# Optimization experiments

Hardware: AMD Instinct MI355X
Metric: run time of the kernel (lower is better)

Reference implementation:

```python
import jax, jax.numpy as jnp
import numpy as np
import math

B, L, D, H = 8, 1000, 1024, 16
HD = D // H

def setup_inputs() -> dict:
    key = jax.random.key(0)
    k1, k2, k3 = jax.random.split(key, 3)
    s_in = 1.0 / math.sqrt(D)
    x = jax.random.normal(k1, (B, L, D), dtype=jnp.float32)
    Wqkv = jax.random.normal(k2, (D, 3 * D), dtype=jnp.float32) * s_in
    bqkv = jnp.zeros((3 * D,), dtype=jnp.float32)
    Wo = jax.random.normal(k3, (D, D), dtype=jnp.float32) * s_in
    bo = jnp.zeros((D,), dtype=jnp.float32)
    return {"x": x, "Wqkv": Wqkv, "bqkv": bqkv, "Wo": Wo, "bo": bo}

def reference(x, Wqkv, bqkv, Wo, bo):
    b, l, d = x.shape
    qkv = x @ Wqkv + bqkv                      # [B,L,3D]
    q, k, v = jnp.split(qkv, 3, axis=-1)       # each [B,L,D]
    q = q.reshape(b, l, H, HD)
    k = k.reshape(b, l, H, HD)
    v = v.reshape(b, l, H, HD)
    scale = 1.0 / math.sqrt(HD)
    att = jnp.einsum('blhd,bmhd->bhlm', q, k) * scale   # [B,H,L,L]
    causal = jnp.tril(jnp.ones((l, l), dtype=bool))      # [L,L]
    att = jnp.where(causal[None, None, :, :], att, -jnp.inf)
    att = jax.nn.softmax(att, axis=-1)
    out = jnp.einsum('bhlm,bmhd->blhd', att, v).reshape(b, l, d)
    return out @ Wo + bo
```

## Files before the change

kernel.cpp:

```cpp
#include <hip/hip_runtime.h>
#include <hip/hip_bf16.h>

typedef unsigned short u16;
typedef unsigned int u32;
typedef __attribute__((ext_vector_type(8))) __bf16 bf16x8;
typedef __attribute__((ext_vector_type(4))) float f32x4;
typedef __attribute__((ext_vector_type(4))) u16 u16x4;

#define LQ 1000
#define MM 8000

__device__ __forceinline__ u16 f2bf(float f){
  __bf16 h = (__bf16)f;
  return __builtin_bit_cast(u16, h);
}
__device__ __forceinline__ void async_copy16(const void* g, void* l){
  __builtin_amdgcn_global_load_lds((const __attribute__((address_space(1))) u32*)g,
                                   (__attribute__((address_space(3))) u32*)l, 16, 0, 0);
}

__global__ __launch_bounds__(256)
void kcvt(const float* __restrict__ src, u16* __restrict__ dst, long n){
  const long i = ((long)blockIdx.x * 256 + threadIdx.x) * 4;
  if (i + 3 >= n) {
    for (long j = i; j < n; j++) dst[j] = f2bf(src[j]);
    return;
  }
  const float4 v = *(const float4*)&src[i];
  u16x4 o; o.x = f2bf(v.x); o.y = f2bf(v.y); o.z = f2bf(v.z); o.w = f2bf(v.w);
  *(u16x4*)&dst[i] = o;
}

__global__ __launch_bounds__(256)
void ktranspose_cvt(const float* __restrict__ src, u16* __restrict__ dst, int R, int C){
  __shared__ u16 tile[32][33];
  const int tx = threadIdx.x & 31, ty = threadIdx.x >> 5;
  const long bx = (long)blockIdx.x * 32, by = (long)blockIdx.y * 32;
  #pragma unroll
  for (int i = 0; i < 32; i += 8) tile[ty + i][tx] = f2bf(src[(by + ty + i) * C + bx + tx]);
  __syncthreads();
  #pragma unroll
  for (int i = 0; i < 32; i += 8) dst[(bx + ty + i) * R + by + tx] = tile[tx][ty + i];
}

template<int EPI>
__global__ __launch_bounds__(512, 2)
void gemm256(const u16* __restrict__ A, const u16* __restrict__ BT, const float* __restrict__ bias,
             u16* __restrict__ O0, u16* __restrict__ O1, u16* __restrict__ O2,
             float* __restrict__ OF)
{
  constexpr int K = 1024;
  constexpr int NT = K / 32;
  extern __shared__ __align__(16) char lds[];
  const int t = threadIdx.x, lane = t & 63, wave = t >> 6;
  const int quad = lane >> 4, l15 = lane & 15;

  const int nwgx = gridDim.x;
  const int nwg = nwgx * gridDim.y;
  int bid = blockIdx.y * nwgx + blockIdx.x;
  bid = (bid & 7) * (nwg >> 3) + (bid >> 3);
  const int m0 = (bid / nwgx) * 256, n0 = (bid % nwgx) * 256;

  const int wm = (wave >> 2) * 128, wn = (wave & 3) * 64;

  const int srow  = wave * 16 + (lane >> 2);
  const int scolg = (lane & 3) ^ ((srow >> 1) & 3);
  const long aofs0 = (long)min(m0 + srow,       MM - 1) * K + scolg * 8;
  const long aofs1 = (long)min(m0 + srow + 128, MM - 1) * K + scolg * 8;
  const long bofs0 = (long)(n0 + srow)       * K + scolg * 8;
  const long bofs1 = (long)(n0 + srow + 128) * K + scolg * 8;

  const int swz = (l15 >> 1) & 3;
  int aoff[8], boff[4];
  #pragma unroll
  for (int m = 0; m < 8; m++) aoff[m] = (wm + m * 16 + l15) * 64 + ((quad ^ swz) << 4);
  #pragma unroll
  for (int n = 0; n < 4; n++) boff[n] = 16384 + (wn + n * 16 + l15) * 64 + ((quad ^ swz) << 4);

  f32x4 acc[8][4] = {};

  auto STAGE_A = [&](int j){
    char* d = lds + (j & 3) * 32768 + wave * 1024;
    const long kt = (long)j * 32;
    async_copy16(A + aofs0 + kt, d);
    async_copy16(A + aofs1 + kt, d + 8192);
  };
  auto STAGE_B = [&](int j){
    char* d = lds + (j & 3) * 32768 + 16384 + wave * 1024;
    const long kt = (long)j * 32;
    async_copy16(BT + bofs0 + kt, d);
    async_copy16(BT + bofs1 + kt, d + 8192);
  };

  STAGE_A(0); STAGE_B(0);
  STAGE_A(1); STAGE_B(1);
  STAGE_A(2); STAGE_B(2);

  for (int j = 0; j < NT; ++j) {
    if (j < NT - 2)       asm volatile("s_waitcnt vmcnt(8)" ::: "memory");
    else if (j == NT - 2) asm volatile("s_waitcnt vmcnt(4)" ::: "memory");
    else                  asm volatile("s_waitcnt vmcnt(0)" ::: "memory");
    __builtin_amdgcn_s_barrier();

    char* buf = lds + (j & 3) * 32768;
    bf16x8 bfr[4], afr[4];
    #pragma unroll
    for (int n = 0; n < 4; n++) bfr[n] = *(const bf16x8*)(buf + boff[n]);
    #pragma unroll
    for (int m = 0; m < 4; m++) afr[m] = *(const bf16x8*)(buf + aoff[m]);
    if (j < NT - 3) STAGE_A(j + 3);

    __builtin_amdgcn_s_setprio(1);
    #pragma unroll
    for (int m = 0; m < 4; m++)
      #pragma unroll
      for (int n = 0; n < 4; n++)
        acc[m][n] = __builtin_amdgcn_mfma_f32_16x16x32_bf16(afr[m], bfr[n], acc[m][n], 0, 0, 0);
    __builtin_amdgcn_s_setprio(0);
    __builtin_amdgcn_s_barrier();

    #pragma unroll
    for (int m = 0; m < 4; m++) afr[m] = *(const bf16x8*)(buf + aoff[m + 4]);
    if (j < NT - 3) STAGE_B(j + 3);

    __builtin_amdgcn_s_setprio(1);
    #pragma unroll
    for (int m = 0; m < 4; m++)
      #pragma unroll
      for (int n = 0; n < 4; n++)
        acc[m + 4][n] = __builtin_amdgcn_mfma_f32_16x16x32_bf16(afr[m], bfr[n], acc[m + 4][n], 0, 0, 0);
    __builtin_amdgcn_s_setprio(0);

    asm volatile("s_waitcnt lgkmcnt(0)" ::: "memory");
  }

  float bs[4]; int cols[4];
  #pragma unroll
  for (int n = 0; n < 4; n++) { cols[n] = n0 + wn + n * 16 + l15; bs[n] = bias[cols[n]]; }

  #pragma unroll
  for (int m = 0; m < 8; m++) {
    #pragma unroll
    for (int r = 0; r < 4; r++) {
      const int row = m0 + wm + m * 16 + quad * 4 + r;
      if (row >= MM) continue;
      if (EPI == 0) {
        const int b = row / 1000, l = row - b * 1000;
        #pragma unroll
        for (int n = 0; n < 4; n++) {
          const u16 o = f2bf(acc[m][n][r] + bs[n]);
          const int col = cols[n];
          const int which = col >> 10, hh = (col >> 6) & 15, dd = col & 63;
          const int bh = b * 16 + hh;
          if      (which == 0) O0[((long)bh * LQ + l) * 64 + dd] = o;
          else if (which == 1) O1[((long)bh * LQ + l) * 64 + dd] = o;
          else                 O2[((long)bh * 64 + dd) * LQ + l] = o;
        }
      } else {
        #pragma unroll
        for (int n = 0; n < 4; n++)
          OF[(long)row * 1024 + cols[n]] = acc[m][n][r] + bs[n];
      }
    }
  }
}

__global__ __launch_bounds__(256)
void attn_kernel(const u16* __restrict__ Qb, const u16* __restrict__ Kb,
                 const u16* __restrict__ VTb, u16* __restrict__ AO)
{
  __shared__ __align__(16) u16 Ps[4][2][16 * 40];
  const int t = threadIdx.x, lane = t & 63, wave = t >> 6;
  const int quad = lane >> 4, l15 = lane & 15;
  const int bh = blockIdx.y;
  const int c = blockIdx.x * 4 + wave;
  const u16* Q  = Qb  + (long)bh * LQ * 64;
  const u16* Kp = Kb  + (long)bh * LQ * 64;
  const u16* VT = VTb + (long)bh * 64 * LQ;
  const int b = bh >> 4, h = bh & 15;
  const float sscale = 0.18033688011112042f;

  for (int pass = 0; pass < 2; ++pass) {
    const int chunk = pass ? (31 - c) : c;
    const int qbase = chunk * 32;
    const int nkt = chunk + 1;

    int qv[2]; bf16x8 bq0[2], bq1[2];
    #pragma unroll
    for (int g = 0; g < 2; g++) {
      qv[g] = qbase + g * 16 + l15;
      const int qc = min(qv[g], LQ - 1);
      bq0[g] = *(const bf16x8*)&Q[(long)qc * 64 +      quad * 8];
      bq1[g] = *(const bf16x8*)&Q[(long)qc * 64 + 32 + quad * 8];
    }

    float l_p[2] = { 0.f, 0.f };
    f32x4 o[2][4] = {};

    bf16x8 pa00, pa01, pa10, pa11, pav0, pav1, pav2, pav3;
    {
      const int krA = min(l15, LQ - 1), krB = min(16 + l15, LQ - 1);
      pa00 = *(const bf16x8*)&Kp[(long)krA * 64 +      quad * 8];
      pa01 = *(const bf16x8*)&Kp[(long)krA * 64 + 32 + quad * 8];
      pa10 = *(const bf16x8*)&Kp[(long)krB * 64 +      quad * 8];
      pa11 = *(const bf16x8*)&Kp[(long)krB * 64 + 32 + quad * 8];
      const int vcol = min(quad * 8, LQ - 8);
      pav0 = *(const bf16x8*)&VT[(long)( 0 + l15) * LQ + vcol];
      pav1 = *(const bf16x8*)&VT[(long)(16 + l15) * LQ + vcol];
      pav2 = *(const bf16x8*)&VT[(long)(32 + l15) * LQ + vcol];
      pav3 = *(const bf16x8*)&VT[(long)(48 + l15) * LQ + vcol];
    }

    for (int kk = 0; kk < nkt; ++kk) {
      const int k0 = kk * 32;
      const bool lastt = (kk + 1 == nkt);
      const bf16x8 a00 = pa00, a01 = pa01, a10 = pa10, a11 = pa11;
      bf16x8 av[4] = { pav0, pav1, pav2, pav3 };
      if (!lastt) {
        const int n0k = k0 + 32;
        const int krA = min(n0k + l15, LQ - 1), krB = min(n0k + 16 + l15, LQ - 1);
        pa00 = *(const bf16x8*)&Kp[(long)krA * 64 +      quad * 8];
        pa01 = *(const bf16x8*)&Kp[(long)krA * 64 + 32 + quad * 8];
        pa10 = *(const bf16x8*)&Kp[(long)krB * 64 +      quad * 8];
        pa11 = *(const bf16x8*)&Kp[(long)krB * 64 + 32 + quad * 8];
        const int vcol = min(n0k + quad * 8, LQ - 8);
        pav0 = *(const bf16x8*)&VT[(long)( 0 + l15) * LQ + vcol];
        pav1 = *(const bf16x8*)&VT[(long)(16 + l15) * LQ + vcol];
        pav2 = *(const bf16x8*)&VT[(long)(32 + l15) * LQ + vcol];
        pav3 = *(const bf16x8*)&VT[(long)(48 + l15) * LQ + vcol];
      }

      #pragma unroll
      for (int g = 0; g < 2; g++) {
        const f32x4 z = {};
        f32x4 s0 = __builtin_amdgcn_mfma_f32_16x16x32_bf16(a00, bq0[g], z, 0, 0, 0);
        s0       = __builtin_amdgcn_mfma_f32_16x16x32_bf16(a01, bq1[g], s0, 0, 0, 0);
        f32x4 s1 = __builtin_amdgcn_mfma_f32_16x16x32_bf16(a10, bq0[g], z, 0, 0, 0);
        s1       = __builtin_amdgcn_mfma_f32_16x16x32_bf16(a11, bq1[g], s1, 0, 0, 0);

        float p0[4], p1[4];
        if (lastt) {
          const int q = qv[g];
          #pragma unroll
          for (int r = 0; r < 4; r++) {
            const int key0 = k0 + quad * 4 + r;
            p0[r] = __builtin_amdgcn_exp2f((key0      <= q) ? s0[r] * sscale : -3.0e38f);
            p1[r] = __builtin_amdgcn_exp2f((key0 + 16 <= q) ? s1[r] * sscale : -3.0e38f);
          }
        } else {
          #pragma unroll
          for (int r = 0; r < 4; r++) {
            p0[r] = __builtin_amdgcn_exp2f(s0[r] * sscale);
            p1[r] = __builtin_amdgcn_exp2f(s1[r] * sscale);
          }
        }
        u16x4 w0, w1; float ls = 0.f;
        #pragma unroll
        for (int r = 0; r < 4; r++) {
          w0[r] = f2bf(p0[r]); w1[r] = f2bf(p1[r]);
          ls += p0[r] + p1[r];
        }
        l_p[g] += ls;
        *(u16x4*)&Ps[wave][g][l15 * 40 + quad * 4]      = w0;
        *(u16x4*)&Ps[wave][g][l15 * 40 + 16 + quad * 4] = w1;
        const bf16x8 bp = *(const bf16x8*)&Ps[wave][g][l15 * 40 + quad * 8];
        #pragma unroll
        for (int cc = 0; cc < 4; cc++)
          o[g][cc] = __builtin_amdgcn_mfma_f32_16x16x32_bf16(av[cc], bp, o[g][cc], 0, 0, 0);
      }
    }

    #pragma unroll
    for (int g = 0; g < 2; g++) {
      if (qv[g] >= LQ) continue;
      float l = l_p[g];
      l += __shfl_xor(l, 16);
      l += __shfl_xor(l, 32);
      const float inv = 1.0f / l;
      const long base = ((long)(b * LQ + qv[g])) * 1024 + h * 64;
      #pragma unroll
      for (int cc = 0; cc < 4; cc++) {
        u16x4 w;
        #pragma unroll
        for (int r = 0; r < 4; r++) w[r] = f2bf(o[g][cc][r] * inv);
        *(u16x4*)&AO[base + cc * 16 + quad * 4] = w;
      }
    }
  }
}

extern "C" void kernel_launch(void* const* d_in, const int* in_sizes, int n_in,
                              void* d_out, int out_size, void* d_ws, size_t ws_size,
                              hipStream_t stream) {
  const float* x    = (const float*)d_in[0];
  const float* Wqkv = (const float*)d_in[1];
  const float* bqkv = (const float*)d_in[2];
  const float* Wo   = (const float*)d_in[3];
  const float* bo   = (const float*)d_in[4];
  float* out = (float*)d_out;

  char* ws = (char*)d_ws;
  u16* WqkvT = (u16*)(ws);
  u16* WoT   = (u16*)(ws + 6291456);
  u16* xb    = (u16*)(ws + 8388608);
  u16* Qb    = (u16*)(ws + 8388608 + 16384000L);
  u16* Kb    = (u16*)(ws + 8388608 + 2 * 16384000L);
  u16* VTb   = (u16*)(ws + 8388608 + 3 * 16384000L);
  u16* AO    = xb;

  static bool inited = false;
  if (!inited) {
    (void)hipFuncSetAttribute(reinterpret_cast<const void*>(&gemm256<0>),
                              hipFuncAttributeMaxDynamicSharedMemorySize, 131072);
    (void)hipFuncSetAttribute(reinterpret_cast<const void*>(&gemm256<1>),
                              hipFuncAttributeMaxDynamicSharedMemorySize, 131072);
    inited = true;
  }

  kcvt<<<8000, 256, 0, stream>>>(x, xb, 8192000L);
  ktranspose_cvt<<<dim3(96, 32), 256, 0, stream>>>(Wqkv, WqkvT, 1024, 3072);
  ktranspose_cvt<<<dim3(32, 32), 256, 0, stream>>>(Wo,   WoT,   1024, 1024);
  gemm256<0><<<dim3(12, 32), 512, 131072, stream>>>(xb, WqkvT, bqkv, Qb, Kb, VTb, nullptr);
  attn_kernel<<<dim3(4, 128), 256, 0, stream>>>(Qb, Kb, VTb, AO);
  gemm256<1><<<dim3(4, 32), 512, 131072, stream>>>(AO, WoT, bo, nullptr, nullptr, nullptr, out);
}
```

Baseline: 276.0 us.

## Template GEMM on N tile, use 256x128 tiles for output projection, restructure barriers

The GEMM kernel gets a template parameter for N tile width. The output projection now runs with 256x128 tiles, doubling its grid from 128 to 256 workgroups so more of the GPU's compute units have work. The main loop is reorganised so the vmcnt wait sits at the end of each iteration, with extra barriers pinned by sched_barrier between the LDS fragment loads and the MFMA phases. The extra barriers per iteration may add synchronisation cost, and the smaller B tile gives less reuse per loaded A tile.

```diff
diff --git a/kernel.cpp b/kernel.cpp
--- a/kernel.cpp
+++ b/kernel.cpp
@@ -17,6 +17,17 @@
 __device__ __forceinline__ void async_copy16(const void* g, void* l){
   __builtin_amdgcn_global_load_lds((const __attribute__((address_space(1))) u32*)g,
                                    (__attribute__((address_space(3))) u32*)l, 16, 0, 0);
+}
+template<int N> __device__ __forceinline__ void wait_vm(){
+  if constexpr (N==8)      asm volatile("s_waitcnt vmcnt(8)" ::: "memory");
+  else if constexpr (N==6) asm volatile("s_waitcnt vmcnt(6)" ::: "memory");
+  else if constexpr (N==4) asm volatile("s_waitcnt vmcnt(4)" ::: "memory");
+  else if constexpr (N==3) asm volatile("s_waitcnt vmcnt(3)" ::: "memory");
+  else                     asm volatile("s_waitcnt vmcnt(0)" ::: "memory");
+}
+__device__ __forceinline__ void barrier_pin(){
+  asm volatile("s_barrier" ::: "memory");
+  __builtin_amdgcn_sched_barrier(0);
 }
 
 __global__ __launch_bounds__(256)
@@ -43,14 +54,16 @@
   for (int i = 0; i < 32; i += 8) dst[(bx + ty + i) * R + by + tx] = tile[tx][ty + i];
 }
 
-template<int EPI>
+template<int EPI, int BN>
 __global__ __launch_bounds__(512, 2)
-void gemm256(const u16* __restrict__ A, const u16* __restrict__ BT, const float* __restrict__ bias,
-             u16* __restrict__ O0, u16* __restrict__ O1, u16* __restrict__ O2,
-             float* __restrict__ OF)
+void gemm8p(const u16* __restrict__ A, const u16* __restrict__ BT, const float* __restrict__ bias,
+            u16* __restrict__ O0, u16* __restrict__ O1, u16* __restrict__ O2,
+            float* __restrict__ OF)
 {
-  constexpr int K = 1024;
-  constexpr int NT = K / 32;
+  constexpr int K = 1024, NT = K / 32;
+  constexpr int NF = BN / 64;
+  constexpr int BUFSZ = 16384 + BN * 64;
+  constexpr int PT = 2 + BN / 128;
   extern __shared__ __align__(16) char lds[];
   const int t = threadIdx.x, lane = t & 63, wave = t >> 6;
   const int quad = lane >> 4, l15 = lane & 15;
@@ -59,84 +72,82 @@
   const int nwg = nwgx * gridDim.y;
   int bid = blockIdx.y * nwgx + blockIdx.x;
   bid = (bid & 7) * (nwg >> 3) + (bid >> 3);
-  const int m0 = (bid / nwgx) * 256, n0 = (bid % nwgx) * 256;
-
-  const int wm = (wave >> 2) * 128, wn = (wave & 3) * 64;
-
-  const int srow  = wave * 16 + (lane >> 2);
-  const int scolg = (lane & 3) ^ ((srow >> 1) & 3);
-  const long aofs0 = (long)min(m0 + srow,       MM - 1) * K + scolg * 8;
-  const long aofs1 = (long)min(m0 + srow + 128, MM - 1) * K + scolg * 8;
-  const long bofs0 = (long)(n0 + srow)       * K + scolg * 8;
-  const long bofs1 = (long)(n0 + srow + 128) * K + scolg * 8;
+  const int m0 = (bid / nwgx) * 256, n0 = (bid % nwgx) * BN;
+
+  const int wm = (wave >> 2) * 128, wn = (wave & 3) * (BN / 4);
+
+  const int srow = t >> 2;
+  const int sg   = (t & 3) ^ ((srow >> 1) & 3);
+  const long aofs0 = (long)min(m0 + srow,       MM - 1) * K + sg * 8;
+  const long aofs1 = (long)min(m0 + srow + 128, MM - 1) * K + sg * 8;
+  const long bofs0 = (long)(n0 + srow) * K + sg * 8;
+  const long bofs1 = (long)(n0 + srow + 128) * K + sg * 8;
 
   const int swz = (l15 >> 1) & 3;
-  int aoff[8], boff[4];
-  #pragma unroll
-  for (int m = 0; m < 8; m++) aoff[m] = (wm + m * 16 + l15) * 64 + ((quad ^ swz) << 4);
-  #pragma unroll
-  for (int n = 0; n < 4; n++) boff[n] = 16384 + (wn + n * 16 + l15) * 64 + ((quad ^ swz) << 4);
-
-  f32x4 acc[8][4] = {};
+  int aoff[8], boff[NF];
+  #pragma unroll
+  for (int m = 0; m < 8; m++)  aoff[m] = (wm + m * 16 + l15) * 64 + ((quad ^ swz) << 4);
+  #pragma unroll
+  for (int n = 0; n < NF; n++) boff[n] = 16384 + (wn + n * 16 + l15) * 64 + ((quad ^ swz) << 4);
+
+  f32x4 acc[8][NF] = {};
 
   auto STAGE_A = [&](int j){
-    char* d = lds + (j & 3) * 32768 + wave * 1024;
+    char* d = lds + (j & 3) * BUFSZ + wave * 1024;
     const long kt = (long)j * 32;
     async_copy16(A + aofs0 + kt, d);
     async_copy16(A + aofs1 + kt, d + 8192);
   };
   auto STAGE_B = [&](int j){
-    char* d = lds + (j & 3) * 32768 + 16384 + wave * 1024;
+    char* d = lds + (j & 3) * BUFSZ + 16384 + wave * 1024;
     const long kt = (long)j * 32;
     async_copy16(BT + bofs0 + kt, d);
-    async_copy16(BT + bofs1 + kt, d + 8192);
+    if constexpr (BN == 256) async_copy16(BT + bofs1 + kt, d + 8192);
   };
 
   STAGE_A(0); STAGE_B(0);
   STAGE_A(1); STAGE_B(1);
   STAGE_A(2); STAGE_B(2);
+  wait_vm<2 * PT>();
+  barrier_pin();
 
   for (int j = 0; j < NT; ++j) {
-    if (j < NT - 2)       asm volatile("s_waitcnt vmcnt(8)" ::: "memory");
-    else if (j == NT - 2) asm volatile("s_waitcnt vmcnt(4)" ::: "memory");
-    else                  asm volatile("s_waitcnt vmcnt(0)" ::: "memory");
-    __builtin_amdgcn_s_barrier();
-
-    char* buf = lds + (j & 3) * 32768;
-    bf16x8 bfr[4], afr[4];
-    #pragma unroll
-    for (int n = 0; n < 4; n++) bfr[n] = *(const bf16x8*)(buf + boff[n]);
-    #pragma unroll
-    for (int m = 0; m < 4; m++) afr[m] = *(const bf16x8*)(buf + aoff[m]);
-    if (j < NT - 3) STAGE_A(j + 3);
-
+    char* buf = lds + (j & 3) * BUFSZ;
+    bf16x8 bfr[NF], afr[4];
+    #pragma unroll
+    for (int n = 0; n < NF; n++) bfr[n] = *(const bf16x8*)(buf + boff[n]);
+    #pragma unroll
+    for (int m = 0; m < 4; m++)  afr[m] = *(const bf16x8*)(buf + aoff[m]);
+    if (j + 3 < NT) STAGE_A(j + 3);
+    barrier_pin();
     __builtin_amdgcn_s_setprio(1);
     #pragma unroll
     for (int m = 0; m < 4; m++)
       #pragma unroll
-      for (int n = 0; n < 4; n++)
+      for (int n = 0; n < NF; n++)
         acc[m][n] = __builtin_amdgcn_mfma_f32_16x16x32_bf16(afr[m], bfr[n], acc[m][n], 0, 0, 0);
     __builtin_amdgcn_s_setprio(0);
-    __builtin_amdgcn_s_barrier();
-
-    #pragma unroll
-    for (int m = 0; m < 4; m++) afr[m] = *(const bf16x8*)(buf + aoff[m + 4]);
-    if (j < NT - 3) STAGE_B(j + 3);
-
+    barrier_pin();
+    #pragma unroll
+    for (int m = 0; m < 4; m++)  afr[m] = *(const bf16x8*)(buf + aoff[4 + m]);
+    if (j + 3 < NT) STAGE_B(j + 3);
+    barrier_pin();
     __builtin_amdgcn_s_setprio(1);
     #pragma unroll
     for (int m = 0; m < 4; m++)
       #pragma unroll
-      for (int n = 0; n < 4; n++)
-        acc[m + 4][n] = __builtin_amdgcn_mfma_f32_16x16x32_bf16(afr[m], bfr[n], acc[m + 4][n], 0, 0, 0);
+      for (int n = 0; n < NF; n++)
+        acc[4 + m][n] = __builtin_amdgcn_mfma_f32_16x16x32_bf16(afr[m], bfr[n], acc[4 + m][n], 0, 0, 0);
     __builtin_amdgcn_s_setprio(0);
-
-    asm volatile("s_waitcnt lgkmcnt(0)" ::: "memory");
-  }
-
-  float bs[4]; int cols[4];
-  #pragma unroll
-  for (int n = 0; n < 4; n++) { cols[n] = n0 + wn + n * 16 + l15; bs[n] = bias[cols[n]]; }
+    if (j <= NT - 4)      wait_vm<2 * PT>();
+    else if (j == NT - 3) wait_vm<PT>();
+    else if (j == NT - 2) wait_vm<0>();
+    barrier_pin();
+  }
+
+  float bs[NF]; int cols[NF];
+  #pragma unroll
+  for (int n = 0; n < NF; n++) { cols[n] = n0 + wn + n * 16 + l15; bs[n] = bias[cols[n]]; }
 
   #pragma unroll
   for (int m = 0; m < 8; m++) {
@@ -147,7 +158,7 @@
       if (EPI == 0) {
         const int b = row / 1000, l = row - b * 1000;
         #pragma unroll
-        for (int n = 0; n < 4; n++) {
+        for (int n = 0; n < NF; n++) {
           const u16 o = f2bf(acc[m][n][r] + bs[n]);
           const int col = cols[n];
           const int which = col >> 10, hh = (col >> 6) & 15, dd = col & 63;
@@ -158,7 +169,7 @@
         }
       } else {
         #pragma unroll
-        for (int n = 0; n < 4; n++)
+        for (int n = 0; n < NF; n++)
           OF[(long)row * 1024 + cols[n]] = acc[m][n][r] + bs[n];
       }
     }
@@ -310,17 +321,17 @@
 
   static bool inited = false;
   if (!inited) {
-    (void)hipFuncSetAttribute(reinterpret_cast<const void*>(&gemm256<0>),
+    (void)hipFuncSetAttribute(reinterpret_cast<const void*>(&gemm8p<0, 256>),
                               hipFuncAttributeMaxDynamicSharedMemorySize, 131072);
-    (void)hipFuncSetAttribute(reinterpret_cast<const void*>(&gemm256<1>),
-                              hipFuncAttributeMaxDynamicSharedMemorySize, 131072);
+    (void)hipFuncSetAttribute(reinterpret_cast<const void*>(&gemm8p<1, 128>),
+                              hipFuncAttributeMaxDynamicSharedMemorySize, 98304);
     inited = true;
   }
 
   kcvt<<<8000, 256, 0, stream>>>(x, xb, 8192000L);
   ktranspose_cvt<<<dim3(96, 32), 256, 0, stream>>>(Wqkv, WqkvT, 1024, 3072);
   ktranspose_cvt<<<dim3(32, 32), 256, 0, stream>>>(Wo,   WoT,   1024, 1024);
-  gemm256<0><<<dim3(12, 32), 512, 131072, stream>>>(xb, WqkvT, bqkv, Qb, Kb, VTb, nullptr);
+  gemm8p<0, 256><<<dim3(12, 32), 512, 131072, stream>>>(xb, WqkvT, bqkv, Qb, Kb, VTb, nullptr);
   attn_kernel<<<dim3(4, 128), 256, 0, stream>>>(Qb, Kb, VTb, AO);
-  gemm256<1><<<dim3(4, 32), 512, 131072, stream>>>(AO, WoT, bo, nullptr, nullptr, nullptr, out);
-}
+  gemm8p<1, 128><<<dim3(8, 32), 512, 98304, stream>>>(AO, WoT, bo, nullptr, nullptr, nullptr, out);
+}
```

Result: no change. 270.8 us (-1.9%).
